# Kernel optimization log

Measured on AMD Instinct MI355X. Metric: run time of the kernel, lower is better.

The kernel has to match this reference:

```python
import jax, jax.numpy as jnp
import numpy as np

EMBED_DIM = 512
N_HEADS = 8
HEAD_DIM = EMBED_DIM // N_HEADS
MAX_GENES = 5000
SPARSITY_RATIO = 0.1
WINDOW = 20  # SparseAttention local window


def make_sparse_mask(key):
    # local band |i-j| <= window//2, plus random connections, plus diagonal
    idx = jnp.arange(MAX_GENES)
    mask = jnp.abs(idx[:, None] - idx[None, :]) <= (WINDOW // 2)
    n_random = int(SPARSITY_RATIO * MAX_GENES * MAX_GENES)
    k1, k2 = jax.random.split(key)
    ri = jax.random.randint(k1, (n_random,), 0, MAX_GENES)
    rj = jax.random.randint(k2, (n_random,), 0, MAX_GENES)
    mask = mask.at[ri, rj].set(True)
    mask = mask.at[idx, idx].set(True)
    return mask  # bool [MAX_GENES, MAX_GENES]


def setup_inputs() -> dict:
    key = jax.random.key(0)
    ks = jax.random.split(key, 10)
    B, S, E = 1, 4096, EMBED_DIM
    x = jax.random.normal(ks[0], (B, S, E), dtype=jnp.float32)
    init = lambda k: jax.random.normal(k, (E, E), dtype=jnp.float32) * 0.02
    return {
        "x": x,
        "Wq": init(ks[1]), "bq": jnp.zeros((E,), jnp.float32),
        "Wk": init(ks[2]), "bk": jnp.zeros((E,), jnp.float32),
        "Wv": init(ks[3]), "bv": jnp.zeros((E,), jnp.float32),
        "Wo": init(ks[4]), "bo": jnp.zeros((E,), jnp.float32),
        "mask": make_sparse_mask(ks[5]),
    }


def reference(x, Wq, bq, Wk, bk, Wv, bv, Wo, bo, mask):
    B, S, E = x.shape
    H, D = N_HEADS, HEAD_DIM
    # QKV projections (torch Linear: x @ W.T + b), split heads -> [B,H,S,D]
    Q = (x @ Wq.T + bq).reshape(B, S, H, D).transpose(0, 2, 1, 3)
    K = (x @ Wk.T + bk).reshape(B, S, H, D).transpose(0, 2, 1, 3)
    V = (x @ Wv.T + bv).reshape(B, S, H, D).transpose(0, 2, 1, 3)
    scale = 1.0 / jnp.sqrt(jnp.asarray(D, dtype=jnp.float32))
    scores = jnp.einsum('bhsd,bhtd->bhst', Q, K) * scale
    m = mask[:S, :S]  # static sparse pattern
    # original: scores*mask then masked_fill(mask==0, -inf) -> equivalent where
    scores = jnp.where(m[None, None], scores, -jnp.inf)
    w = jax.nn.softmax(scores, axis=-1)
    w = jnp.nan_to_num(w, nan=0.0)  # diag is always unmasked, but keep faithful
    out = jnp.einsum('bhst,bhtd->bhsd', w, V)
    out = out.transpose(0, 2, 1, 3).reshape(B, S, E)
    return out @ Wo.T + bo
```

## Files before the change

kernel.cpp:

```cpp
#include <hip/hip_runtime.h>
#include <hip/hip_bf16.h>
#include <stdint.h>

#define S 4096
#define E 512
#define H 8
#define D 64
#define MROW 5000

typedef __hip_bfloat16 bf16;
typedef __attribute__((ext_vector_type(8))) short bf16x8;
typedef __attribute__((ext_vector_type(4))) float f32x4;

#define CMUL (0.125f * 1.4426950408889634f)

__global__ __launch_bounds__(256) void prep(
    const void* __restrict__ mask, unsigned long long* __restrict__ bitsT,
    const float* __restrict__ x,  const float* __restrict__ wq,
    const float* __restrict__ wk, const float* __restrict__ wv,
    const float* __restrict__ wo, const float* __restrict__ bq,
    const float* __restrict__ bk, const float* __restrict__ bv,
    const float* __restrict__ bo,
    bf16* __restrict__ xb, bf16* __restrict__ wcat, bf16* __restrict__ wob,
    bf16* __restrict__ bcat, bf16* __restrict__ bob)
{
    const int tid = threadIdx.x;
    const int b   = blockIdx.x;
    const int gid = b * 256 + tid;
    for (int g = gid; g < 786944; g += 524288) {
        const float* src; bf16* dst; int e;
        if (g < 524288) { src = x; dst = xb; e = g * 4; }
        else {
            int r = g - 524288;
            if      (r < 65536)  { src = wq; dst = wcat;          e = r * 4; }
            else if (r < 131072) { src = wk; dst = wcat + 262144; e = (r - 65536) * 4; }
            else if (r < 196608) { src = wv; dst = wcat + 524288; e = (r - 131072) * 4; }
            else if (r < 262144) { src = wo; dst = wob;           e = (r - 196608) * 4; }
            else if (r < 262272) { src = bq; dst = bcat;          e = (r - 262144) * 4; }
            else if (r < 262400) { src = bk; dst = bcat + 512;    e = (r - 262272) * 4; }
            else if (r < 262528) { src = bv; dst = bcat + 1024;   e = (r - 262400) * 4; }
            else                 { src = bo; dst = bob;           e = (r - 262528) * 4; }
        }
        float4 v = *(const float4*)(src + e);
        union { bf16 h[4]; uint2 u; } cv;
        cv.h[0] = (bf16)v.x; cv.h[1] = (bf16)v.y;
        cv.h[2] = (bf16)v.z; cv.h[3] = (bf16)v.w;
        *(uint2*)(dst + e) = cv.u;
    }
    {
        const unsigned int* mw32 = (const unsigned int*)mask;
        int lane = tid & 63;
        int hit = 0;
#pragma unroll
        for (int i = 0; i < 8; ++i) {
            unsigned int w = mw32[lane + i * 64];
            if (w > 1u && (w & 0xFEFEFEFEu) == 0u) hit = 1;
        }
        const bool isbyte = (__ballot(hit) != 0ull);
        int wid  = (b * 256 + tid) >> 6;
        int nwav = (2048 * 256) >> 6;
        int total = (S / 64) * S;
        for (int w = wid; w < total; w += nwav) {
            int word = w >> 12;
            int row  = w & (S - 1);
            int col  = word * 64 + lane;
            unsigned int v;
            if (isbyte) v = ((const unsigned char*)mask)[(size_t)row * MROW + col];
            else        v = ((const unsigned int*)mask)[(size_t)row * MROW + col];
            unsigned long long bb = __ballot(v != 0u);
            if (lane == 0) bitsT[(size_t)word * S + row] = bb;
        }
    }
}

__global__ __launch_bounds__(256) void gemm_qkv(const bf16* __restrict__ A,
                                                const bf16* __restrict__ W,
                                                const bf16* __restrict__ bias,
                                                bf16* __restrict__ out)
{
    __shared__ bf16 As[128][72];
    __shared__ bf16 Bs[64][72];
    const int tid  = threadIdx.x;
    const int wid  = tid >> 6, lane = tid & 63;
    const int quad = lane >> 4, l15 = lane & 15;
    const int nbase = blockIdx.x * 64;
    const int mbase = blockIdx.y * 128;
    const int wr = wid * 32;

    f32x4 acc[2][4];
#pragma unroll
    for (int i = 0; i < 2; ++i)
#pragma unroll
        for (int j = 0; j < 4; ++j) acc[i][j] = (f32x4){0.f, 0.f, 0.f, 0.f};

    for (int kt = 0; kt < E / 64; ++kt) {
        const int kb = kt * 64;
        __syncthreads();
#pragma unroll
        for (int i = 0; i < 4; ++i) {
            int slot = tid + i * 256;
            int row = slot >> 3, kg = slot & 7;
            *(uint4*)&As[row][kg * 8] = *(const uint4*)&A[(size_t)(mbase + row) * E + kb + kg * 8];
        }
#pragma unroll
        for (int i = 0; i < 2; ++i) {
            int slot = tid + i * 256;
            int row = slot >> 3, kg = slot & 7;
            *(uint4*)&Bs[row][kg * 8] = *(const uint4*)&W[(size_t)(nbase + row) * E + kb + kg * 8];
        }
        __syncthreads();
        bf16x8 a0[2], a1[2];
#pragma unroll
        for (int mt = 0; mt < 2; ++mt) {
            a0[mt] = *(bf16x8*)&As[wr + mt * 16 + l15][quad * 8];
            a1[mt] = *(bf16x8*)&As[wr + mt * 16 + l15][32 + quad * 8];
        }
#pragma unroll
        for (int nt = 0; nt < 4; ++nt) {
            bf16x8 b0 = *(bf16x8*)&Bs[nt * 16 + l15][quad * 8];
            bf16x8 b1 = *(bf16x8*)&Bs[nt * 16 + l15][32 + quad * 8];
#pragma unroll
            for (int mt = 0; mt < 2; ++mt) {
                acc[mt][nt] = __builtin_amdgcn_mfma_f32_16x16x32_bf16(a0[mt], b0, acc[mt][nt], 0, 0, 0);
                acc[mt][nt] = __builtin_amdgcn_mfma_f32_16x16x32_bf16(a1[mt], b1, acc[mt][nt], 0, 0, 0);
            }
        }
    }
#pragma unroll
    for (int nt = 0; nt < 4; ++nt) {
        int col = nbase + nt * 16 + l15;
        float bv = (float)bias[col];
        int t = col >> 9, hh = (col >> 6) & 7, d = col & 63;
#pragma unroll
        for (int mt = 0; mt < 2; ++mt)
#pragma unroll
            for (int r = 0; r < 4; ++r) {
                int row = mbase + wr + mt * 16 + quad * 4 + r;
                float v = acc[mt][nt][r] + bv;
                if (t == 0) v *= CMUL;
                out[((size_t)t * H + hh) * S * D + (size_t)row * D + d] = (bf16)v;
            }
    }
}

__global__ __launch_bounds__(256) void attn(const bf16* __restrict__ Qp,
                                            const bf16* __restrict__ Kp,
                                            const bf16* __restrict__ Vp,
                                            const unsigned long long* __restrict__ bitsT,
                                            float* __restrict__ Opart,
                                            float* __restrict__ Lpart,
                                            int ktper)
{
    __shared__ __align__(16) char smem[32768];
    bf16 (*Ps)[32][64] = (bf16(*)[32][64])smem;
    bf16 (*Ks)[64]     = (bf16(*)[64])(smem + 16384);
    bf16 (*Vts)[64]    = (bf16(*)[64])(smem + 24576);

    const int tid  = threadIdx.x;
    const int wid  = tid >> 6, lane = tid & 63;
    const int quad = lane >> 4, l15 = lane & 15;
    const int qb = blockIdx.x, h = blockIdx.y, split = blockIdx.z;
    const int qbase = qb * 128;
    const int m0 = wid * 32;
    const bf16* Qh = Qp + (size_t)h * S * D;
    const bf16* Kh = Kp + (size_t)h * S * D;
    const bf16* Vh = Vp + (size_t)h * S * D;

    const int krow0 = tid >> 3, kkg = tid & 7;
    const int krow1 = (tid + 256) >> 3;
    const int ksw0 = (kkg ^ (krow0 & 7)) * 8;
    const int ksw1 = (kkg ^ (krow1 & 7)) * 8;
    const int vt0 = (tid & 31) * 2, vd0 = (tid >> 5) * 8;

    const bf16* qr0 = Qh + (size_t)(qbase + m0 + l15) * D;
    bf16x8 aq00 = *(const bf16x8*)(qr0 + quad * 8);
    bf16x8 aq01 = *(const bf16x8*)(qr0 + 32 + quad * 8);
    bf16x8 aq10 = *(const bf16x8*)(qr0 + 16 * D + quad * 8);
    bf16x8 aq11 = *(const bf16x8*)(qr0 + 16 * D + 32 + quad * 8);

    bf16x8 bl;
    {
        union { short s; bf16 b; } one; one.b = (bf16)1.0f;
        short v = (l15 == 0) ? one.s : (short)0;
#pragma unroll
        for (int j = 0; j < 8; ++j) bl[j] = v;
    }

    f32x4 o[4][2];
#pragma unroll
    for (int dt = 0; dt < 4; ++dt)
#pragma unroll
        for (int u = 0; u < 2; ++u) o[dt][u] = (f32x4){0.f, 0.f, 0.f, 0.f};
    f32x4 accl[2];
    accl[0] = (f32x4){0.f, 0.f, 0.f, 0.f};
    accl[1] = (f32x4){0.f, 0.f, 0.f, 0.f};

    const int kt0 = split * ktper, kt1 = kt0 + ktper;

    const bf16* kp0 = Kh + (size_t)(kt0 * 64 + krow0) * D + kkg * 8;
    const bf16* kp1 = Kh + (size_t)(kt0 * 64 + krow1) * D + kkg * 8;
    const bf16* vp0 = Vh + (size_t)(kt0 * 64 + vt0) * D + vd0;
    const bf16* vp1 = Vh + (size_t)(kt0 * 64 + vt0 + 1) * D + vd0;
    uint4 kq0 = *(const uint4*)kp0;
    uint4 kq1 = *(const uint4*)kp1;
    uint4 vq0 = *(const uint4*)vp0;
    uint4 vq1 = *(const uint4*)vp1;

    const unsigned long long* mb0 = bitsT + (size_t)kt0 * S + qbase + m0 + l15;
    const unsigned long long* mb1 = mb0 + 16;

    const int ksw_rd = (l15 & 7);
#pragma unroll 1
    for (int kt = kt0; kt < kt1; ++kt) {
        __syncthreads();
        *(uint4*)&Ks[krow0][ksw0] = kq0;
        *(uint4*)&Ks[krow1][ksw1] = kq1;
        {
            const unsigned int* w0 = (const unsigned int*)&vq0;
            const unsigned int* w1 = (const unsigned int*)&vq1;
#pragma unroll
            for (int j = 0; j < 8; ++j) {
                unsigned int pk = __builtin_amdgcn_perm(
                    w1[j >> 1], w0[j >> 1],
                    (j & 1) ? 0x07060302u : 0x05040100u);
                *(unsigned int*)&Vts[vd0 + j][vt0 ^ (j * 8)] = pk;
            }
        }
        if (kt + 1 < kt1) {
            kp0 += 64 * D; kp1 += 64 * D; vp0 += 64 * D; vp1 += 64 * D;
            kq0 = *(const uint4*)kp0;
            kq1 = *(const uint4*)kp1;
            vq0 = *(const uint4*)vp0;
            vq1 = *(const uint4*)vp1;
        }
        unsigned long long mw0 = *mb0; mb0 += S;
        unsigned long long mw1 = *mb1; mb1 += S;
        __syncthreads();

        f32x4 sc[2][4];
        {
            f32x4 z = (f32x4){0.f, 0.f, 0.f, 0.f};
            __builtin_amdgcn_s_setprio(1);
#pragma unroll
            for (int nt = 0; nt < 4; ++nt) {
                bf16x8 kb0 = *(bf16x8*)&Ks[nt * 16 + l15][(quad ^ ksw_rd) * 8];
                bf16x8 kb1 = *(bf16x8*)&Ks[nt * 16 + l15][((quad + 4) ^ ksw_rd) * 8];
                sc[0][nt] = __builtin_amdgcn_mfma_f32_16x16x32_bf16(kb0, aq00, z, 0, 0, 0);
                sc[0][nt] = __builtin_amdgcn_mfma_f32_16x16x32_bf16(kb1, aq01, sc[0][nt], 0, 0, 0);
                sc[1][nt] = __builtin_amdgcn_mfma_f32_16x16x32_bf16(kb0, aq10, z, 0, 0, 0);
                sc[1][nt] = __builtin_amdgcn_mfma_f32_16x16x32_bf16(kb1, aq11, sc[1][nt], 0, 0, 0);
            }
            __builtin_amdgcn_s_setprio(0);
        }
#pragma unroll
        for (int u = 0; u < 2; ++u) {
            const unsigned long long sh = (u ? mw1 : mw0) >> (quad * 4);
            const unsigned int wlo = (unsigned int)sh;
            const unsigned int whi = (unsigned int)(sh >> 32);
#pragma unroll
            for (int nt = 0; nt < 4; ++nt) {
                const unsigned int wsel = (nt < 2) ? wlo : whi;
                unsigned int a[4];
#pragma unroll
                for (int r = 0; r < 4; ++r) {
                    const int bit = (nt & 1) * 16 + r;
                    unsigned int m = (unsigned int)((int)(wsel << (31 - bit)) >> 31);
                    a[r] = (__float_as_uint(__builtin_amdgcn_exp2f(sc[u][nt][r])) & m) + 0x8000u;
                }
                uint2 pk;
                pk.x = __builtin_amdgcn_perm(a[1], a[0], 0x07060302u);
                pk.y = __builtin_amdgcn_perm(a[3], a[2], 0x07060302u);
                *(uint2*)&Ps[wid][u * 16 + l15][(nt * 16 + quad * 4) ^ (ksw_rd * 8)] = pk;
            }
        }
        bf16x8 ap00 = *(bf16x8*)&Ps[wid][l15][(quad * 8) ^ (ksw_rd * 8)];
        bf16x8 ap01 = *(bf16x8*)&Ps[wid][l15][(32 + quad * 8) ^ (ksw_rd * 8)];
        bf16x8 ap10 = *(bf16x8*)&Ps[wid][16 + l15][(quad * 8) ^ (ksw_rd * 8)];
        bf16x8 ap11 = *(bf16x8*)&Ps[wid][16 + l15][(32 + quad * 8) ^ (ksw_rd * 8)];
        __builtin_amdgcn_s_setprio(1);
        accl[0] = __builtin_amdgcn_mfma_f32_16x16x32_bf16(ap00, bl, accl[0], 0, 0, 0);
        accl[0] = __builtin_amdgcn_mfma_f32_16x16x32_bf16(ap01, bl, accl[0], 0, 0, 0);
        accl[1] = __builtin_amdgcn_mfma_f32_16x16x32_bf16(ap10, bl, accl[1], 0, 0, 0);
        accl[1] = __builtin_amdgcn_mfma_f32_16x16x32_bf16(ap11, bl, accl[1], 0, 0, 0);
#pragma unroll
        for (int dt = 0; dt < 4; ++dt) {
            bf16x8 bv0 = *(bf16x8*)&Vts[dt * 16 + l15][(quad ^ ksw_rd) * 8];
            bf16x8 bv1 = *(bf16x8*)&Vts[dt * 16 + l15][((quad + 4) ^ ksw_rd) * 8];
            o[dt][0] = __builtin_amdgcn_mfma_f32_16x16x32_bf16(ap00, bv0, o[dt][0], 0, 0, 0);
            o[dt][0] = __builtin_amdgcn_mfma_f32_16x16x32_bf16(ap01, bv1, o[dt][0], 0, 0, 0);
            o[dt][1] = __builtin_amdgcn_mfma_f32_16x16x32_bf16(ap10, bv0, o[dt][1], 0, 0, 0);
            o[dt][1] = __builtin_amdgcn_mfma_f32_16x16x32_bf16(ap11, bv1, o[dt][1], 0, 0, 0);
        }
        __builtin_amdgcn_s_setprio(0);
    }
    float* Op = Opart + (size_t)(split * H + h) * S * D;
    float* Lp = Lpart + (size_t)(split * H + h) * S;
#pragma unroll
    for (int u = 0; u < 2; ++u)
#pragma unroll
        for (int r = 0; r < 4; ++r) {
            int row = qbase + m0 + u * 16 + quad * 4 + r;
            if (l15 == 0) Lp[row] = accl[u][r];
#pragma unroll
            for (int dt = 0; dt < 4; ++dt)
                Op[(size_t)row * D + dt * 16 + l15] = o[dt][u][r];
        }
}

__global__ __launch_bounds__(256) void combine(const float* __restrict__ Opart,
                                               const float* __restrict__ Lpart,
                                               bf16* __restrict__ Ab, int nsplit)
{
    const size_t oh = (size_t)H * S * D;
    int g = blockIdx.x * 256 + threadIdx.x;
    int row = g >> 6;
    int cg  = g & 63;
    int hh  = cg >> 3;
    int d0  = (cg & 7) * 8;
    size_t base = ((size_t)hh * S + row) * D + d0;
    float a[8] = {0.f, 0.f, 0.f, 0.f, 0.f, 0.f, 0.f, 0.f};
    float l = 0.f;
    for (int s = 0; s < nsplit; ++s) {
        float4 p0 = *(const float4*)(Opart + (size_t)s * oh + base);
        float4 p1 = *(const float4*)(Opart + (size_t)s * oh + base + 4);
        a[0] += p0.x; a[1] += p0.y; a[2] += p0.z; a[3] += p0.w;
        a[4] += p1.x; a[5] += p1.y; a[6] += p1.z; a[7] += p1.w;
        l += Lpart[(size_t)s * H * S + (size_t)hh * S + row];
    }
    float inv = (l > 0.f) ? 1.f / l : 0.f;
    union { bf16 hb[8]; uint4 u; } cv;
#pragma unroll
    for (int j = 0; j < 8; ++j) cv.hb[j] = (bf16)(a[j] * inv);
    *(uint4*)&Ab[(size_t)row * E + hh * 64 + d0] = cv.u;
}

__global__ __launch_bounds__(256) void gemm_out(const bf16* __restrict__ A,
                                                const bf16* __restrict__ W,
                                                const bf16* __restrict__ bias,
                                                float* __restrict__ out)
{
    __shared__ bf16 As[128][72];
    __shared__ bf16 Bs[64][72];
    const int tid  = threadIdx.x;
    const int wid  = tid >> 6, lane = tid & 63;
    const int quad = lane >> 4, l15 = lane & 15;
    const int nbase = blockIdx.x * 64;
    const int mbase = blockIdx.y * 128;
    const int wr = wid * 32;

    f32x4 acc[2][4];
#pragma unroll
    for (int i = 0; i < 2; ++i)
#pragma unroll
        for (int j = 0; j < 4; ++j) acc[i][j] = (f32x4){0.f, 0.f, 0.f, 0.f};

    for (int kt = 0; kt < E / 64; ++kt) {
        const int kb = kt * 64;
        __syncthreads();
#pragma unroll
        for (int i = 0; i < 4; ++i) {
            int slot = tid + i * 256;
            int row = slot >> 3, kg = slot & 7;
            *(uint4*)&As[row][kg * 8] = *(const uint4*)&A[(size_t)(mbase + row) * E + kb + kg * 8];
        }
#pragma unroll
        for (int i = 0; i < 2; ++i) {
            int slot = tid + i * 256;
            int row = slot >> 3, kg = slot & 7;
            *(uint4*)&Bs[row][kg * 8] = *(const uint4*)&W[(size_t)(nbase + row) * E + kb + kg * 8];
        }
        __syncthreads();
        bf16x8 a0[2], a1[2];
#pragma unroll
        for (int mt = 0; mt < 2; ++mt) {
            a0[mt] = *(bf16x8*)&As[wr + mt * 16 + l15][quad * 8];
            a1[mt] = *(bf16x8*)&As[wr + mt * 16 + l15][32 + quad * 8];
        }
#pragma unroll
        for (int nt = 0; nt < 4; ++nt) {
            bf16x8 b0 = *(bf16x8*)&Bs[nt * 16 + l15][quad * 8];
            bf16x8 b1 = *(bf16x8*)&Bs[nt * 16 + l15][32 + quad * 8];
#pragma unroll
            for (int mt = 0; mt < 2; ++mt) {
                acc[mt][nt] = __builtin_amdgcn_mfma_f32_16x16x32_bf16(a0[mt], b0, acc[mt][nt], 0, 0, 0);
                acc[mt][nt] = __builtin_amdgcn_mfma_f32_16x16x32_bf16(a1[mt], b1, acc[mt][nt], 0, 0, 0);
            }
        }
    }
#pragma unroll
    for (int nt = 0; nt < 4; ++nt) {
        int col = nbase + nt * 16 + l15;
        float bv = (float)bias[col];
#pragma unroll
        for (int mt = 0; mt < 2; ++mt)
#pragma unroll
            for (int r = 0; r < 4; ++r) {
                int row = mbase + wr + mt * 16 + quad * 4 + r;
                out[(size_t)row * E + col] = acc[mt][nt][r] + bv;
            }
    }
}

extern "C" void kernel_launch(void* const* d_in, const int* in_sizes, int n_in,
                              void* d_out, int out_size, void* d_ws, size_t ws_size,
                              hipStream_t stream)
{
    char* ws = (char*)d_ws;
    const size_t MB = (size_t)1 << 20;
    bf16* Qw   = (bf16*)(ws + 0 * MB);
    bf16* Kw   = (bf16*)(ws + 4 * MB);
    bf16* Vw   = (bf16*)(ws + 8 * MB);
    bf16* Ab   = (bf16*)(ws + 12 * MB);
    unsigned long long* bitsT = (unsigned long long*)(ws + 16 * MB);
    bf16* xb   = (bf16*)(ws + 18 * MB);
    bf16* Wcat = (bf16*)(ws + 22 * MB);
    bf16* Wob  = (bf16*)(ws + 24 * MB);
    bf16* bcat = (bf16*)(ws + 25 * MB);
    bf16* bob  = (bf16*)(ws + 25 * MB + 8192);
    float* Opart = (float*)(ws + 26 * MB);

    int nsplit = (ws_size >= 59 * MB) ? 4 : 2;
    int ktper  = (S / 64) / nsplit;
    float* Lpart = (float*)(ws + 26 * MB + (size_t)nsplit * 8 * MB);

    hipLaunchKernelGGL(prep, dim3(2048), dim3(256), 0, stream,
                       d_in[9], bitsT,
                       (const float*)d_in[0], (const float*)d_in[1],
                       (const float*)d_in[3], (const float*)d_in[5],
                       (const float*)d_in[7], (const float*)d_in[2],
                       (const float*)d_in[4], (const float*)d_in[6],
                       (const float*)d_in[8],
                       xb, Wcat, Wob, bcat, bob);
    hipLaunchKernelGGL(gemm_qkv, dim3(24, 32), dim3(256), 0, stream,
                       xb, Wcat, bcat, Qw);
    hipLaunchKernelGGL(attn, dim3(S / 128, H, nsplit), dim3(256), 0, stream,
                       Qw, Kw, Vw, bitsT, Opart, Lpart, ktper);
    hipLaunchKernelGGL(combine, dim3(1024), dim3(256), 0, stream,
                       Opart, Lpart, Ab, nsplit);
    hipLaunchKernelGGL(gemm_out, dim3(8, 32), dim3(256), 0, stream,
                       Ab, Wob, bob, (float*)d_out);
}
```

Measured before the change: 272.4 us.

## Fuse split-K combine into attention via last-block atomic counter

Drops the separate combine kernel. Each attention block bumps a per-query-block atomic counter after writing its partial output, and the last of the H*nsplit blocks for that query block reduces the partials and writes the normalized bf16 attention output. The intent is to save one kernel launch and let the combine overlap with attention blocks still running. The cost is a threadfence plus an atomic in every block, and a serialized reduction tail carried by only 32 blocks. The counters are zeroed in prep.

```diff
diff --git a/kernel.cpp b/kernel.cpp
--- a/kernel.cpp
+++ b/kernel.cpp
@@ -22,10 +22,12 @@
     const float* __restrict__ bk, const float* __restrict__ bv,
     const float* __restrict__ bo,
     bf16* __restrict__ xb, bf16* __restrict__ wcat, bf16* __restrict__ wob,
-    bf16* __restrict__ bcat, bf16* __restrict__ bob)
+    bf16* __restrict__ bcat, bf16* __restrict__ bob,
+    unsigned int* __restrict__ cnt)
 {
     const int tid = threadIdx.x;
     const int b   = blockIdx.x;
+    if (b == 0 && tid < 32) cnt[tid] = 0u;
     const int gid = b * 256 + tid;
     for (int g = gid; g < 786944; g += 524288) {
         const float* src; bf16* dst; int e;
@@ -149,6 +151,8 @@
                                             const unsigned long long* __restrict__ bitsT,
                                             float* __restrict__ Opart,
                                             float* __restrict__ Lpart,
+                                            bf16* __restrict__ Ab,
+                                            unsigned int* __restrict__ cnt,
                                             int ktper)
 {
     __shared__ __align__(16) char smem[32768];
@@ -305,33 +309,42 @@
             for (int dt = 0; dt < 4; ++dt)
                 Op[(size_t)row * D + dt * 16 + l15] = o[dt][u][r];
         }
-}
-
-__global__ __launch_bounds__(256) void combine(const float* __restrict__ Opart,
-                                               const float* __restrict__ Lpart,
-                                               bf16* __restrict__ Ab, int nsplit)
-{
-    const size_t oh = (size_t)H * S * D;
-    int g = blockIdx.x * 256 + threadIdx.x;
-    int row = g >> 6;
-    int cg  = g & 63;
-    int hh  = cg >> 3;
-    int d0  = (cg & 7) * 8;
-    size_t base = ((size_t)hh * S + row) * D + d0;
-    float a[8] = {0.f, 0.f, 0.f, 0.f, 0.f, 0.f, 0.f, 0.f};
-    float l = 0.f;
-    for (int s = 0; s < nsplit; ++s) {
-        float4 p0 = *(const float4*)(Opart + (size_t)s * oh + base);
-        float4 p1 = *(const float4*)(Opart + (size_t)s * oh + base + 4);
-        a[0] += p0.x; a[1] += p0.y; a[2] += p0.z; a[3] += p0.w;
-        a[4] += p1.x; a[5] += p1.y; a[6] += p1.z; a[7] += p1.w;
-        l += Lpart[(size_t)s * H * S + (size_t)hh * S + row];
-    }
-    float inv = (l > 0.f) ? 1.f / l : 0.f;
-    union { bf16 hb[8]; uint4 u; } cv;
-#pragma unroll
-    for (int j = 0; j < 8; ++j) cv.hb[j] = (bf16)(a[j] * inv);
-    *(uint4*)&Ab[(size_t)row * E + hh * 64 + d0] = cv.u;
+
+    const int nsplit = (S / 64) / ktper;
+    __threadfence();
+    __syncthreads();
+    if (tid == 0) *(volatile int*)smem = (int)atomicAdd(&cnt[qb], 1u);
+    __syncthreads();
+    if (*(volatile int*)smem == H * nsplit - 1) {
+        __threadfence();
+        const size_t oh = (size_t)H * S * D;
+#pragma unroll 1
+        for (int it = 0; it < 32; ++it) {
+            int g = it * 256 + tid;
+            int row = qbase + (g >> 6);
+            int cg  = g & 63;
+            int hh  = cg >> 3;
+            int d0  = (cg & 7) * 8;
+            size_t base = ((size_t)hh * S + row) * D + d0;
+            float a[8] = {0.f, 0.f, 0.f, 0.f, 0.f, 0.f, 0.f, 0.f};
+            float l = 0.f;
+#pragma unroll
+            for (int s = 0; s < 4; ++s) {
+                if (s >= nsplit) break;
+                float4 p0 = *(const float4*)(Opart + (size_t)s * oh + base);
+                float4 p1 = *(const float4*)(Opart + (size_t)s * oh + base + 4);
+                a[0] += p0.x; a[1] += p0.y; a[2] += p0.z; a[3] += p0.w;
+                a[4] += p1.x; a[5] += p1.y; a[6] += p1.z; a[7] += p1.w;
+                l += Lpart[(size_t)s * H * S + (size_t)hh * S + row];
+            }
+            float inv = (l > 0.f) ? 1.f / l : 0.f;
+            union { bf16 hb[8]; uint4 u; } cv;
+#pragma unroll
+            for (int j = 0; j < 8; ++j) cv.hb[j] = (bf16)(a[j] * inv);
+            *(uint4*)&Ab[(size_t)row * E + cg * 8] = cv.u;
+        }
+        if (tid == 0) cnt[qb] = 0u;
+    }
 }
 
 __global__ __launch_bounds__(256) void gemm_out(const bf16* __restrict__ A,
@@ -417,6 +430,7 @@
     bf16* Wob  = (bf16*)(ws + 24 * MB);
     bf16* bcat = (bf16*)(ws + 25 * MB);
     bf16* bob  = (bf16*)(ws + 25 * MB + 8192);
+    unsigned int* cnt = (unsigned int*)(ws + 25 * MB + 32768);
     float* Opart = (float*)(ws + 26 * MB);
 
     int nsplit = (ws_size >= 59 * MB) ? 4 : 2;
@@ -430,13 +444,11 @@
                        (const float*)d_in[7], (const float*)d_in[2],
                        (const float*)d_in[4], (const float*)d_in[6],
                        (const float*)d_in[8],
-                       xb, Wcat, Wob, bcat, bob);
+                       xb, Wcat, Wob, bcat, bob, cnt);
     hipLaunchKernelGGL(gemm_qkv, dim3(24, 32), dim3(256), 0, stream,
                        xb, Wcat, bcat, Qw);
     hipLaunchKernelGGL(attn, dim3(S / 128, H, nsplit), dim3(256), 0, stream,
-                       Qw, Kw, Vw, bitsT, Opart, Lpart, ktper);
-    hipLaunchKernelGGL(combine, dim3(1024), dim3(256), 0, stream,
-                       Opart, Lpart, Ab, nsplit);
+                       Qw, Kw, Vw, bitsT, Opart, Lpart, Ab, cnt, ktper);
     hipLaunchKernelGGL(gemm_out, dim3(8, 32), dim3(256), 0, stream,
                        Ab, Wob, bob, (float*)d_out);
 }
```

New measurement: 440.8 us. 61.8% more time.
